# Optimization experiments

Measured on AMD Instinct MI355X. Metric: run time of the kernel, lower is better.

The kernel has to match this reference:

```python
import jax, jax.numpy as jnp
import numpy as np

N, D, H, R = 50000, 256, 4, 3
C = D // H        # head dim = 64
E = 400000        # edges per relation
NEG = 0.2         # LeakyReLU slope
LN_EPS = 1e-5


def _segment_softmax(att, seg, n):
    # att: [E, H], seg: [E] destination node ids -> softmax per (node, head)
    m = jax.ops.segment_max(att, seg, num_segments=n)
    m = jnp.where(jnp.isfinite(m), m, 0.0)        # nodes with no edges
    e = jnp.exp(att - m[seg])
    s = jax.ops.segment_sum(e, seg, num_segments=n)
    return e / (s[seg] + 1e-16)


def setup_inputs() -> dict:
    key = jax.random.key(0)
    ks = jax.random.split(key, 16)
    inp = {
        'feat': jax.random.normal(ks[0], (N, D), jnp.float32),
        'Wl': jax.random.normal(ks[1], (D, D), jnp.float32) / np.sqrt(D).astype(np.float32),
        'bl': jnp.zeros((D,), jnp.float32),
        'Wr': jax.random.normal(ks[2], (D, D), jnp.float32) / np.sqrt(D).astype(np.float32),
        'br': jnp.zeros((D,), jnp.float32),
        'attn_l': jax.random.normal(ks[3], (R, H, C), jnp.float32) / np.sqrt(C).astype(np.float32),
        'attn_r': jax.random.normal(ks[4], (R, H, C), jnp.float32) / np.sqrt(C).astype(np.float32),
        'rel_q': jax.random.normal(ks[5], (H, C), jnp.float32) / np.sqrt(C).astype(np.float32),
        'rel_k': jax.random.normal(ks[6], (H, C), jnp.float32) / np.sqrt(C).astype(np.float32),
        'ln_gamma': jnp.ones((D,), jnp.float32),
        'ln_beta': jnp.zeros((D,), jnp.float32),
    }
    for r in range(R):
        inp[f'edge_src_{r}'] = jax.random.randint(ks[7 + 2 * r], (E,), 0, N, jnp.int64 if jax.config.jax_enable_x64 else jnp.int32)
        inp[f'edge_dst_{r}'] = jax.random.randint(ks[8 + 2 * r], (E,), 0, N, jnp.int64 if jax.config.jax_enable_x64 else jnp.int32)
    return inp


def reference(feat, Wl, bl, Wr, br, attn_l, attn_r, rel_q, rel_k, ln_gamma, ln_beta,
              edge_src_0, edge_dst_0, edge_src_1, edge_dst_1, edge_src_2, edge_dst_2):
    # per-node-type linear projections -> multi-head [N, H, C]
    k = (feat @ Wl + bl).reshape(N, H, C)
    v = (feat @ Wr + br).reshape(N, H, C)
    srcs = [edge_src_0, edge_src_1, edge_src_2]
    dsts = [edge_dst_0, edge_dst_1, edge_dst_2]
    rel_outs = []
    for r in range(R):  # loop over fixed, structurally distinct relations
        s, d = srcs[r], dsts[r]
        # edge attention: (k_src . a_l) + (v_dst . a_r), LeakyReLU (attn_dropout inactive in eval)
        att = jnp.einsum('ehc,hc->eh', k[s], attn_l[r]) + jnp.einsum('ehc,hc->eh', v[d], attn_r[r])
        att = jax.nn.leaky_relu(att, NEG)
        a = _segment_softmax(att, d, N)                                   # [E, H]
        # message 'h' is edges.dst['v'] in the original code (faithful)
        h = jax.ops.segment_sum(a[:, :, None] * v[d], d, num_segments=N)  # [N, H, C]
        rel_outs.append(h)
    # stack relation embeddings + self 'v' (the +1 none-selection relation)
    x = jnp.stack(rel_outs + [v], axis=1)                                  # [N, T=R+1, H, C]
    # MetapathGATConv (1 layer) stand-in: self embedding queries all relations per head
    q = jnp.einsum('nhc,hc->nh', x[:, -1], rel_q)                          # [N, H]
    kk = jnp.einsum('nthc,hc->nth', x, rel_k)                              # [N, T, H]
    beta = jax.nn.softmax(jax.nn.leaky_relu(q[:, None, :] + kk, NEG), axis=1)  # [N, T, H]
    out = jnp.einsum('nth,nthc->nhc', beta, x).reshape(N, D)
    # activation -> (dropout inactive in eval) -> LayerNorm
    out = jax.nn.relu(out)
    mu = out.mean(-1, keepdims=True)
    var = out.var(-1, keepdims=True)
    out = (out - mu) * jax.lax.rsqrt(var + LN_EPS) * ln_gamma + ln_beta
    return out
```

## Files before the change

kernel.cpp:

```cpp
#include <hip/hip_runtime.h>

#define N_NODES 50000
#define DIM 256
#define NEG 0.2f
#define LN_EPS 1e-5f
#define SCAT_BLOCKS 2048

typedef __attribute__((ext_vector_type(8))) short short8;
typedef __attribute__((ext_vector_type(4))) float f32x4;

__device__ __forceinline__ unsigned short f2bf(float x) {
    unsigned int u = __builtin_bit_cast(unsigned int, x);
    u += 0x7fffu + ((u >> 16) & 1u);
    return (unsigned short)(u >> 16);
}

__device__ __forceinline__ void load_lds16(const void* g, void* l) {
    __builtin_amdgcn_global_load_lds((const unsigned int*)g, (unsigned int*)l, 16, 0, 0);
}

__global__ __launch_bounds__(256) void prep(
    const float* __restrict__ Wr, unsigned short* __restrict__ WrF,
    const int* __restrict__ d0, const int* __restrict__ d1, const int* __restrict__ d2,
    int E, unsigned char* __restrict__ mask)
{
    if (blockIdx.x < 32) {
        const int o    = blockIdx.x * 256 + threadIdx.x;
        const int lane = o & 63;
        const int frag = o >> 6;
        const int kk = frag & 7, mt = frag >> 3;
        const int ln = lane & 15, quad = lane >> 4;
        const float* src = Wr + (size_t)(kk * 32 + quad * 8) * DIM + mt * 16 + ln;
        short8 v;
        #pragma unroll
        for (int j = 0; j < 8; ++j) v[j] = (short)f2bf(src[(size_t)j * DIM]);
        *(short8*)(WrF + (size_t)o * 8) = v;
    } else {
        const int total = 3 * E;
        for (int i = (blockIdx.x - 32) * 256 + (int)threadIdx.x; i < total;
             i += SCAT_BLOCKS * 256) {
            const int* d; int base, e;
            if (i >= 2 * E)  { d = d2; e = i - 2 * E; base = 2 * N_NODES; }
            else if (i >= E) { d = d1; e = i - E;     base = N_NODES; }
            else             { d = d0; e = i;         base = 0; }
            mask[base + d[e]] = (unsigned char)1;
        }
    }
}

__global__ __launch_bounds__(256, 2) void fused_mfma(
    const float* __restrict__ feat, const unsigned short* __restrict__ WrF,
    const float* __restrict__ br, const float* __restrict__ rel_q,
    const float* __restrict__ rel_k, const float* __restrict__ gamma,
    const float* __restrict__ beta_p, const unsigned char* __restrict__ mask,
    float* __restrict__ out)
{
    __shared__ unsigned short lds[32768];
    const int lane = threadIdx.x & 63;
    const int wave = threadIdx.x >> 6;
    const int ln = lane & 15;
    const int quad = lane >> 4;
    int node = blockIdx.x * 64 + wave * 16 + ln;
    const bool valid = node < N_NODES;
    if (!valid) node = N_NODES - 1;

    {
        const char* g = (const char*)WrF;
        #pragma unroll
        for (int r = 0; r < 16; ++r) {
            const int off = wave * 16384 + r * 1024;
            load_lds16(g + off + lane * 16, (char*)lds + off);
        }
    }

    const float* fptr = feat + (size_t)node * DIM + quad * 8;
    float4 F0[8], F1[8];
    #pragma unroll
    for (int kk = 0; kk < 8; ++kk) {
        F0[kk] = *(const float4*)(fptr + kk * 32);
        F1[kk] = *(const float4*)(fptr + kk * 32 + 4);
    }
    short8 bfr[8];
    #pragma unroll
    for (int kk = 0; kk < 8; ++kk) {
        bfr[kk][0] = (short)f2bf(F0[kk].x); bfr[kk][1] = (short)f2bf(F0[kk].y);
        bfr[kk][2] = (short)f2bf(F0[kk].z); bfr[kk][3] = (short)f2bf(F0[kk].w);
        bfr[kk][4] = (short)f2bf(F1[kk].x); bfr[kk][5] = (short)f2bf(F1[kk].y);
        bfr[kk][6] = (short)f2bf(F1[kk].z); bfr[kk][7] = (short)f2bf(F1[kk].w);
    }

    f32x4 acc[16];
    #pragma unroll
    for (int mt = 0; mt < 16; ++mt) acc[mt] = (f32x4){0.f, 0.f, 0.f, 0.f};

    __syncthreads();

    #pragma unroll
    for (int kk = 0; kk < 8; ++kk) {
        #pragma unroll
        for (int mt = 0; mt < 8; ++mt) {
            const short8 a = *(const short8*)((const char*)lds
                               + (mt * 8 + kk) * 1024 + lane * 16);
            acc[mt] = __builtin_amdgcn_mfma_f32_16x16x32_bf16(a, bfr[kk], acc[mt], 0, 0, 0);
        }
    }

    __syncthreads();

    {
        const char* g = (const char*)WrF + 65536;
        #pragma unroll
        for (int r = 0; r < 16; ++r) {
            const int off = wave * 16384 + r * 1024;
            load_lds16(g + off + lane * 16, (char*)lds + off);
        }
    }
    __syncthreads();

    #pragma unroll
    for (int kk = 0; kk < 8; ++kk) {
        #pragma unroll
        for (int mt = 0; mt < 8; ++mt) {
            const short8 a = *(const short8*)((const char*)lds
                               + (mt * 8 + kk) * 1024 + lane * 16);
            acc[8 + mt] = __builtin_amdgcn_mfma_f32_16x16x32_bf16(a, bfr[kk], acc[8 + mt], 0, 0, 0);
        }
    }

    float qp[4] = {0.f, 0.f, 0.f, 0.f}, kp[4] = {0.f, 0.f, 0.f, 0.f};
    #pragma unroll
    for (int mt = 0; mt < 16; ++mt) {
        const int cbase = mt * 16 + quad * 4;
        const float4 bb = *(const float4*)(br + cbase);
        acc[mt][0] += bb.x; acc[mt][1] += bb.y; acc[mt][2] += bb.z; acc[mt][3] += bb.w;
        const float4 rq = *(const float4*)(rel_q + cbase);
        const float4 rk = *(const float4*)(rel_k + cbase);
        const int h = mt >> 2;
        qp[h] += acc[mt][0] * rq.x + acc[mt][1] * rq.y + acc[mt][2] * rq.z + acc[mt][3] * rq.w;
        kp[h] += acc[mt][0] * rk.x + acc[mt][1] * rk.y + acc[mt][2] * rk.z + acc[mt][3] * rk.w;
    }
    #pragma unroll
    for (int h = 0; h < 4; ++h) {
        qp[h] += __shfl_xor(qp[h], 16); qp[h] += __shfl_xor(qp[h], 32);
        kp[h] += __shfl_xor(kp[h], 16); kp[h] += __shfl_xor(kp[h], 32);
    }

    const int cnt = (int)mask[node] + (int)mask[N_NODES + node] + (int)mask[2 * N_NODES + node];

    float wgt[4];
    #pragma unroll
    for (int h = 0; h < 4; ++h) {
        const float q = qp[h];
        const float qk = q + kp[h];
        const float a = q  > 0.f ? q  : NEG * q;
        const float b = qk > 0.f ? qk : NEG * qk;
        const float mx = fmaxf(a, b);
        const float eb = (float)(cnt + 1) * __expf(b - mx);
        const float ea = (float)(3 - cnt) * __expf(a - mx);
        wgt[h] = eb / (eb + ea);
    }

    float sum = 0.f, ssq = 0.f;
    #pragma unroll
    for (int mt = 0; mt < 16; ++mt) {
        const float w = wgt[mt >> 2];
        #pragma unroll
        for (int r = 0; r < 4; ++r) {
            float v = fmaxf(acc[mt][r] * w, 0.f);
            acc[mt][r] = v;
            sum += v; ssq += v * v;
        }
    }
    sum += __shfl_xor(sum, 16); sum += __shfl_xor(sum, 32);
    ssq += __shfl_xor(ssq, 16); ssq += __shfl_xor(ssq, 32);
    const float mu = sum * (1.f / 256.f);
    const float var = ssq * (1.f / 256.f) - mu * mu;
    const float rstd = rsqrtf(var + LN_EPS);

    if (valid) {
        float* optr = out + (size_t)node * DIM;
        #pragma unroll
        for (int mt = 0; mt < 16; ++mt) {
            const int cbase = mt * 16 + quad * 4;
            const float4 g = *(const float4*)(gamma + cbase);
            const float4 b = *(const float4*)(beta_p + cbase);
            float4 r;
            r.x = (acc[mt][0] - mu) * rstd * g.x + b.x;
            r.y = (acc[mt][1] - mu) * rstd * g.y + b.y;
            r.z = (acc[mt][2] - mu) * rstd * g.z + b.z;
            r.w = (acc[mt][3] - mu) * rstd * g.w + b.w;
            *(float4*)(optr + cbase) = r;
        }
    }
}

extern "C" void kernel_launch(void* const* d_in, const int* in_sizes, int n_in,
                              void* d_out, int out_size, void* d_ws, size_t ws_size,
                              hipStream_t stream) {
    const float* feat  = (const float*)d_in[0];
    const float* Wr    = (const float*)d_in[3];
    const float* br    = (const float*)d_in[4];
    const float* rel_q = (const float*)d_in[7];
    const float* rel_k = (const float*)d_in[8];
    const float* gamma = (const float*)d_in[9];
    const float* beta  = (const float*)d_in[10];
    const int* dst0 = (const int*)d_in[12];
    const int* dst1 = (const int*)d_in[14];
    const int* dst2 = (const int*)d_in[16];
    const int E = in_sizes[12];

    unsigned short* WrF = (unsigned short*)d_ws;
    unsigned char* mask = (unsigned char*)d_ws + DIM * DIM * 2;

    hipMemsetAsync(mask, 0, 150016, stream);
    prep<<<32 + SCAT_BLOCKS, 256, 0, stream>>>(Wr, WrF, dst0, dst1, dst2, E, mask);
    fused_mfma<<<(N_NODES + 63) / 64, 256, 0, stream>>>(
        feat, WrF, br, rel_q, rel_k, gamma, beta, mask, (float*)d_out);
}
```

Before: 160.3 us.

## Double-buffer Wr fragment loads into LDS and raise occupancy target

The fused MFMA kernel used to stage the whole bf16 Wr matrix through a 64 KB LDS buffer in two halves, each followed by a full barrier. It now streams Wr in eight 16 KB chunks through a two-slot LDS buffer, issuing the next chunk's async global-to-LDS load while computing on the current one. Halving LDS and raising launch bounds to 4 blocks per CU aim to improve occupancy and latency hiding. The mask reads are also hoisted ahead of the feature loads. The tradeoffs are more barriers and a tighter register budget, which could cause spills given the 64 accumulator registers plus feature fragments.

After: 182.8 us. 14.0% more time.

```diff
diff --git a/kernel.cpp b/kernel.cpp
--- a/kernel.cpp
+++ b/kernel.cpp
@@ -48,14 +48,14 @@
     }
 }
 
-__global__ __launch_bounds__(256, 2) void fused_mfma(
+__global__ __launch_bounds__(256, 4) void fused_mfma(
     const float* __restrict__ feat, const unsigned short* __restrict__ WrF,
     const float* __restrict__ br, const float* __restrict__ rel_q,
     const float* __restrict__ rel_k, const float* __restrict__ gamma,
     const float* __restrict__ beta_p, const unsigned char* __restrict__ mask,
     float* __restrict__ out)
 {
-    __shared__ unsigned short lds[32768];
+    __shared__ unsigned short lds[2][8192];
     const int lane = threadIdx.x & 63;
     const int wave = threadIdx.x >> 6;
     const int ln = lane & 15;
@@ -67,11 +67,15 @@
     {
         const char* g = (const char*)WrF;
         #pragma unroll
-        for (int r = 0; r < 16; ++r) {
-            const int off = wave * 16384 + r * 1024;
-            load_lds16(g + off + lane * 16, (char*)lds + off);
-        }
-    }
+        for (int r = 0; r < 4; ++r) {
+            const int off = wave * 4096 + r * 1024;
+            load_lds16(g + off + lane * 16, (char*)lds[0] + off);
+        }
+    }
+
+    const int m0 = (int)mask[node];
+    const int m1 = (int)mask[N_NODES + node];
+    const int m2 = (int)mask[2 * N_NODES + node];
 
     const float* fptr = feat + (size_t)node * DIM + quad * 8;
     float4 F0[8], F1[8];
@@ -96,35 +100,27 @@
     __syncthreads();
 
     #pragma unroll
-    for (int kk = 0; kk < 8; ++kk) {
-        #pragma unroll
-        for (int mt = 0; mt < 8; ++mt) {
-            const short8 a = *(const short8*)((const char*)lds
-                               + (mt * 8 + kk) * 1024 + lane * 16);
-            acc[mt] = __builtin_amdgcn_mfma_f32_16x16x32_bf16(a, bfr[kk], acc[mt], 0, 0, 0);
-        }
-    }
-
-    __syncthreads();
-
-    {
-        const char* g = (const char*)WrF + 65536;
-        #pragma unroll
-        for (int r = 0; r < 16; ++r) {
-            const int off = wave * 16384 + r * 1024;
-            load_lds16(g + off + lane * 16, (char*)lds + off);
-        }
-    }
-    __syncthreads();
-
-    #pragma unroll
-    for (int kk = 0; kk < 8; ++kk) {
-        #pragma unroll
-        for (int mt = 0; mt < 8; ++mt) {
-            const short8 a = *(const short8*)((const char*)lds
-                               + (mt * 8 + kk) * 1024 + lane * 16);
-            acc[8 + mt] = __builtin_amdgcn_mfma_f32_16x16x32_bf16(a, bfr[kk], acc[8 + mt], 0, 0, 0);
-        }
+    for (int p = 0; p < 8; ++p) {
+        if (p < 7) {
+            const char* g = (const char*)WrF + (p + 1) * 16384;
+            char* l = (char*)lds[(p + 1) & 1];
+            #pragma unroll
+            for (int r = 0; r < 4; ++r) {
+                const int off = wave * 4096 + r * 1024;
+                load_lds16(g + off + lane * 16, l + off);
+            }
+        }
+        const char* b = (const char*)lds[p & 1];
+        #pragma unroll
+        for (int kk = 0; kk < 8; ++kk) {
+            #pragma unroll
+            for (int mtl = 0; mtl < 2; ++mtl) {
+                const short8 a = *(const short8*)(b + (mtl * 8 + kk) * 1024 + lane * 16);
+                acc[p * 2 + mtl] =
+                    __builtin_amdgcn_mfma_f32_16x16x32_bf16(a, bfr[kk], acc[p * 2 + mtl], 0, 0, 0);
+            }
+        }
+        if (p < 7) __syncthreads();
     }
 
     float qp[4] = {0.f, 0.f, 0.f, 0.f}, kp[4] = {0.f, 0.f, 0.f, 0.f};
@@ -145,7 +141,7 @@
         kp[h] += __shfl_xor(kp[h], 16); kp[h] += __shfl_xor(kp[h], 32);
     }
 
-    const int cnt = (int)mask[node] + (int)mask[N_NODES + node] + (int)mask[2 * N_NODES + node];
+    const int cnt = m0 + m1 + m2;
 
     float wgt[4];
     #pragma unroll
```

## Reorder weight fragments by K and overlap second LDS load with MFMA chunk

Applied to the files above, without the earlier changes.

The pre-swizzled bf16 weight layout changes from M-major to K-major, so the GEMM proceeds in K slices across all 16 output tiles. LDS grows to 80 KB so the first 4.x K slices fit. One K slice is computed while the remaining three slices load, which partly hides the second global-to-LDS load behind MFMA work. The mask loads are also hoisted ahead of the feature loads to hide their latency. The larger LDS footprint (80 KB per block) may cut the number of resident blocks per CU.

New measurement: 159.4 us. Within noise of the previous version (-0.6%).

```diff
diff --git a/kernel.cpp b/kernel.cpp
--- a/kernel.cpp
+++ b/kernel.cpp
@@ -17,6 +17,15 @@
 
 __device__ __forceinline__ void load_lds16(const void* g, void* l) {
     __builtin_amdgcn_global_load_lds((const unsigned int*)g, (unsigned int*)l, 16, 0, 0);
+}
+
+__device__ __forceinline__ short8 cvt_bfrag(float4 a4, float4 b4) {
+    short8 r;
+    r[0] = (short)f2bf(a4.x); r[1] = (short)f2bf(a4.y);
+    r[2] = (short)f2bf(a4.z); r[3] = (short)f2bf(a4.w);
+    r[4] = (short)f2bf(b4.x); r[5] = (short)f2bf(b4.y);
+    r[6] = (short)f2bf(b4.z); r[7] = (short)f2bf(b4.w);
+    return r;
 }
 
 __global__ __launch_bounds__(256) void prep(
@@ -28,7 +37,7 @@
         const int o    = blockIdx.x * 256 + threadIdx.x;
         const int lane = o & 63;
         const int frag = o >> 6;
-        const int kk = frag & 7, mt = frag >> 3;
+        const int mt = frag & 15, kk = frag >> 4;
         const int ln = lane & 15, quad = lane >> 4;
         const float* src = Wr + (size_t)(kk * 32 + quad * 8) * DIM + mt * 16 + ln;
         short8 v;
@@ -55,7 +64,7 @@
     const float* __restrict__ beta_p, const unsigned char* __restrict__ mask,
     float* __restrict__ out)
 {
-    __shared__ unsigned short lds[32768];
+    __shared__ unsigned short lds[40960];
     const int lane = threadIdx.x & 63;
     const int wave = threadIdx.x >> 6;
     const int ln = lane & 15;
@@ -71,7 +80,16 @@
             const int off = wave * 16384 + r * 1024;
             load_lds16(g + off + lane * 16, (char*)lds + off);
         }
-    }
+        #pragma unroll
+        for (int r = 0; r < 4; ++r) {
+            const int off = wave * 4096 + r * 1024;
+            load_lds16(g + 65536 + off + lane * 16, (char*)lds + 65536 + off);
+        }
+    }
+
+    const int m0 = (int)mask[node];
+    const int m1 = (int)mask[N_NODES + node];
+    const int m2 = (int)mask[2 * N_NODES + node];
 
     const float* fptr = feat + (size_t)node * DIM + quad * 8;
     float4 F0[8], F1[8];
@@ -82,12 +100,7 @@
     }
     short8 bfr[8];
     #pragma unroll
-    for (int kk = 0; kk < 8; ++kk) {
-        bfr[kk][0] = (short)f2bf(F0[kk].x); bfr[kk][1] = (short)f2bf(F0[kk].y);
-        bfr[kk][2] = (short)f2bf(F0[kk].z); bfr[kk][3] = (short)f2bf(F0[kk].w);
-        bfr[kk][4] = (short)f2bf(F1[kk].x); bfr[kk][5] = (short)f2bf(F1[kk].y);
-        bfr[kk][6] = (short)f2bf(F1[kk].z); bfr[kk][7] = (short)f2bf(F1[kk].w);
-    }
+    for (int kk = 0; kk < 8; ++kk) bfr[kk] = cvt_bfrag(F0[kk], F1[kk]);
 
     f32x4 acc[16];
     #pragma unroll
@@ -96,11 +109,11 @@
     __syncthreads();
 
     #pragma unroll
-    for (int kk = 0; kk < 8; ++kk) {
-        #pragma unroll
-        for (int mt = 0; mt < 8; ++mt) {
+    for (int kk = 0; kk < 4; ++kk) {
+        #pragma unroll
+        for (int mt = 0; mt < 16; ++mt) {
             const short8 a = *(const short8*)((const char*)lds
-                               + (mt * 8 + kk) * 1024 + lane * 16);
+                               + (kk * 16 + mt) * 1024 + lane * 16);
             acc[mt] = __builtin_amdgcn_mfma_f32_16x16x32_bf16(a, bfr[kk], acc[mt], 0, 0, 0);
         }
     }
@@ -108,22 +121,29 @@
     __syncthreads();
 
     {
-        const char* g = (const char*)WrF + 65536;
-        #pragma unroll
-        for (int r = 0; r < 16; ++r) {
-            const int off = wave * 16384 + r * 1024;
+        const char* g = (const char*)WrF + 81920;
+        #pragma unroll
+        for (int r = 0; r < 12; ++r) {
+            const int off = (wave * 12 + r) * 1024;
             load_lds16(g + off + lane * 16, (char*)lds + off);
         }
     }
+    #pragma unroll
+    for (int mt = 0; mt < 16; ++mt) {
+        const short8 a = *(const short8*)((const char*)lds
+                           + 65536 + mt * 1024 + lane * 16);
+        acc[mt] = __builtin_amdgcn_mfma_f32_16x16x32_bf16(a, bfr[4], acc[mt], 0, 0, 0);
+    }
+
     __syncthreads();
 
     #pragma unroll
-    for (int kk = 0; kk < 8; ++kk) {
-        #pragma unroll
-        for (int mt = 0; mt < 8; ++mt) {
+    for (int kk = 5; kk < 8; ++kk) {
+        #pragma unroll
+        for (int mt = 0; mt < 16; ++mt) {
             const short8 a = *(const short8*)((const char*)lds
-                               + (mt * 8 + kk) * 1024 + lane * 16);
-            acc[8 + mt] = __builtin_amdgcn_mfma_f32_16x16x32_bf16(a, bfr[kk], acc[8 + mt], 0, 0, 0);
+                               + ((kk - 5) * 16 + mt) * 1024 + lane * 16);
+            acc[mt] = __builtin_amdgcn_mfma_f32_16x16x32_bf16(a, bfr[kk], acc[mt], 0, 0, 0);
         }
     }
 
@@ -145,7 +165,7 @@
         kp[h] += __shfl_xor(kp[h], 16); kp[h] += __shfl_xor(kp[h], 32);
     }
 
-    const int cnt = (int)mask[node] + (int)mask[N_NODES + node] + (int)mask[2 * N_NODES + node];
+    const int cnt = m0 + m1 + m2;
 
     float wgt[4];
     #pragma unroll
```
